# Optimization experiments

Measured on AMD Instinct MI355X. Metric: run time of the kernel, lower is better.

The kernel has to match this reference:

```python
import jax, jax.numpy as jnp
import numpy as np

D_K = 128

def setup_inputs() -> dict:
    key = jax.random.key(0)
    k1, k2, k3 = jax.random.split(key, 3)
    q = jax.random.normal(k1, (8192, D_K), dtype=jnp.float32)
    k = jax.random.normal(k2, (8192, D_K), dtype=jnp.float32)
    v = jax.random.normal(k3, (8192, D_K), dtype=jnp.float32)
    return {"q": q, "k": k, "v": v}

def reference(q, k, v):
    # scores: [S_q, S_k]
    scores = jnp.einsum('qd,kd->qk', q, k) / jnp.sqrt(jnp.float32(D_K))
    attn = jax.nn.softmax(scores, axis=-1)  # softmax over keys (torch default last dim)
    return jnp.einsum('qk,kd->qd', attn, v)
```

## Files before the change

### kernel.cpp

```cpp
#include <hip/hip_runtime.h>
#include <math.h>


typedef _Float16 f16x8 __attribute__((ext_vector_type(8)));
typedef float    f32x16 __attribute__((ext_vector_type(16)));

constexpr int S_LEN = 8192;
constexpr int D_K   = 128;
constexpr int NSLICE = 8;
constexpr int ITERS2 = (S_LEN / NSLICE) / 64;

constexpr size_t WS_L_OFF = 0;
constexpr size_t KV_OFF   = 262144;
constexpr size_t PART_OFF = KV_OFF + (size_t)256 * 16384;
constexpr size_t WS_NEED  = PART_OFF + (size_t)7 * S_LEN * D_K * 4;

#define CSCALE (0.08838834764831845f * 1.44269504088896340736f)

union UH8 { _Float16 h[8]; uint4 q; f16x8 v; };
union UF4 { unsigned u[4]; uint4 q; f16x8 v; };

__device__ inline void async16(const uint4* g, uint4* l) {
  __builtin_amdgcn_global_load_lds(
      (const __attribute__((address_space(1))) unsigned int*)g,
      (__attribute__((address_space(3))) unsigned int*)l, 16, 0, 0);
}

template <bool ZOUT>
__global__ __launch_bounds__(512) void attn_prep(const float* __restrict__ K,
                                                 const float* __restrict__ V,
                                                 float* __restrict__ out,
                                                 char* __restrict__ ws) {
  const int t = blockIdx.x * 512 + threadIdx.x;
  uint4* KVg = (uint4*)(ws + KV_OFF);
  if (t < 131072) {
    int kt = t >> 9, idx = t & 511;
    int lane = idx & 63, s = idx >> 6;
    int key = kt * 32 + (lane & 31);
    int d0  = s * 16 + (lane >> 5) * 8;
    const float4* src = (const float4*)(K + (size_t)key * D_K + d0);
    float4 a = src[0], b = src[1];
    float f[8] = {a.x, a.y, a.z, a.w, b.x, b.y, b.z, b.w};
    UH8 h;
    #pragma unroll
    for (int j = 0; j < 8; ++j) h.h[j] = (_Float16)f[j];
    KVg[(size_t)kt * 1024 + idx] = h.q;
  } else if (t < 262144) {
    int g = t - 131072;
    int kt = g >> 9, idx = g & 511;
    int lane = idx & 63, c = (idx >> 6) & 3, kstep = idx >> 8;
    int d  = c * 32 + (lane & 31);
    int kb = kt * 32 + kstep * 16 + (lane >> 5) * 8;
    UH8 h;
    #pragma unroll
    for (int j = 0; j < 8; ++j) h.h[j] = (_Float16)V[(size_t)(kb + j) * D_K + d];
    KVg[(size_t)kt * 1024 + 512 + idx] = h.q;
  } else if (ZOUT && t < 327680) {
    int i = t - 262144;
    float4 z = make_float4(0.f, 0.f, 0.f, 0.f);
    float4* o4 = (float4*)out;
    #pragma unroll
    for (int j = 0; j < 4; ++j) o4[(size_t)i * 4 + j] = z;
  } else if (ZOUT && t < 329728) {
    int i = t - 327680;
    ((float4*)(ws + WS_L_OFF))[i] = make_float4(0.f, 0.f, 0.f, 0.f);
  }
}

__device__ inline void softmax32(const f32x16& Sa, const f32x16& Sb,
                                 float& lsum, UF4& A0, UF4& A1) {
  unsigned pk[8];
  #pragma unroll
  for (int i = 0; i < 8; ++i) {
    float p0 = __builtin_amdgcn_exp2f(Sa[2 * i]     + Sb[2 * i]);
    float p1 = __builtin_amdgcn_exp2f(Sa[2 * i + 1] + Sb[2 * i + 1]);
    lsum += p0 + p1;
    pk[i] = __builtin_bit_cast(unsigned, __builtin_amdgcn_cvt_pkrtz(p0, p1));
  }
  auto r0 = __builtin_amdgcn_permlane32_swap((int)pk[0], (int)pk[2], false, false);
  auto r1 = __builtin_amdgcn_permlane32_swap((int)pk[1], (int)pk[3], false, false);
  auto r2 = __builtin_amdgcn_permlane32_swap((int)pk[4], (int)pk[6], false, false);
  auto r3 = __builtin_amdgcn_permlane32_swap((int)pk[5], (int)pk[7], false, false);
  A0.u[0] = (unsigned)r0[0]; A0.u[2] = (unsigned)r0[1];
  A0.u[1] = (unsigned)r1[0]; A0.u[3] = (unsigned)r1[1];
  A1.u[0] = (unsigned)r2[0]; A1.u[2] = (unsigned)r2[1];
  A1.u[1] = (unsigned)r3[0]; A1.u[3] = (unsigned)r3[1];
}

template <bool PARTIAL>
__global__ __launch_bounds__(256, 2)
void attn_main(const float* __restrict__ Qg, float* __restrict__ out,
               char* __restrict__ ws) {
  __shared__ uint4 KV[2][2048];

  const int tid   = threadIdx.x;
  const int wave  = tid >> 6;
  const int lane  = tid & 63;
  const int lrow  = lane & 31;
  const int lhalf = lane >> 5;

  const int blk = blockIdx.x;
  const int ks  = blk & 7;
  const int qb  = blk >> 3;
  const int qw  = qb * 128 + wave * 32;

  {
    const int delay = (int)(((unsigned)blk * 2654435761u) >> 28);
    for (int i = 0; i < delay; ++i) __builtin_amdgcn_s_sleep(2);
  }

  float* ws_l = (float*)(ws + WS_L_OFF);

  f16x8 qf[8];
  {
    const int q = qw + lrow;
    #pragma unroll
    for (int s = 0; s < 8; ++s) {
      const float4* src = (const float4*)(Qg + (size_t)q * D_K + s * 16 + lhalf * 8);
      float4 a = src[0], b = src[1];
      float f[8] = {a.x, a.y, a.z, a.w, b.x, b.y, b.z, b.w};
      UH8 h;
      #pragma unroll
      for (int j = 0; j < 8; ++j) h.h[j] = (_Float16)(f[j] * CSCALE);
      qf[s] = h.v;
    }
  }

  f32x16 O0{}, O1{}, O2{}, O3{};
  float lsum = 0.f;

  const uint4* KVg = (const uint4*)(ws + KV_OFF);

  {
    const size_t base = (size_t)ks * 32768;
    #pragma unroll
    for (int i = 0; i < 8; ++i)
      async16(KVg + base + i * 256 + tid, &KV[0][i * 256 + tid]);
  }

  for (int it = 0; it < ITERS2; ++it) {
    const int buf = it & 1;
    __syncthreads();

    if (it + 1 < ITERS2) {
      const size_t base = (size_t)ks * 32768 + (size_t)(it + 1) * 2048;
      #pragma unroll
      for (int i = 0; i < 8; ++i)
        async16(KVg + base + i * 256 + tid, &KV[buf ^ 1][i * 256 + tid]);
    }

    const uint4* sub0 = &KV[buf][0];
    const uint4* sub1 = &KV[buf][1024];

    f32x16 Sa0{}, Sb0{}, Sa1{}, Sb1{};
    __builtin_amdgcn_s_setprio(1);
    #pragma unroll
    for (int s = 0; s < 4; ++s) {
      f16x8 ka0 = __builtin_bit_cast(f16x8, sub0[(2 * s    ) * 64 + lane]);
      f16x8 kb0 = __builtin_bit_cast(f16x8, sub0[(2 * s + 1) * 64 + lane]);
      Sa0 = __builtin_amdgcn_mfma_f32_32x32x16_f16(ka0, qf[2 * s    ], Sa0, 0, 0, 0);
      Sb0 = __builtin_amdgcn_mfma_f32_32x32x16_f16(kb0, qf[2 * s + 1], Sb0, 0, 0, 0);
    }
    #pragma unroll
    for (int s = 0; s < 4; ++s) {
      f16x8 ka1 = __builtin_bit_cast(f16x8, sub1[(2 * s    ) * 64 + lane]);
      f16x8 kb1 = __builtin_bit_cast(f16x8, sub1[(2 * s + 1) * 64 + lane]);
      Sa1 = __builtin_amdgcn_mfma_f32_32x32x16_f16(ka1, qf[2 * s    ], Sa1, 0, 0, 0);
      Sb1 = __builtin_amdgcn_mfma_f32_32x32x16_f16(kb1, qf[2 * s + 1], Sb1, 0, 0, 0);
    }
    __builtin_amdgcn_s_setprio(0);

    UF4 A00, A01;
    softmax32(Sa0, Sb0, lsum, A00, A01);

    __builtin_amdgcn_s_setprio(1);
    #pragma unroll
    for (int kstep = 0; kstep < 2; ++kstep) {
      f16x8 pf = kstep ? A01.v : A00.v;
      f16x8 v0 = __builtin_bit_cast(f16x8, sub0[512 + kstep * 256 +   0 + lane]);
      f16x8 v1 = __builtin_bit_cast(f16x8, sub0[512 + kstep * 256 +  64 + lane]);
      f16x8 v2 = __builtin_bit_cast(f16x8, sub0[512 + kstep * 256 + 128 + lane]);
      f16x8 v3 = __builtin_bit_cast(f16x8, sub0[512 + kstep * 256 + 192 + lane]);
      O0 = __builtin_amdgcn_mfma_f32_32x32x16_f16(pf, v0, O0, 0, 0, 0);
      O1 = __builtin_amdgcn_mfma_f32_32x32x16_f16(pf, v1, O1, 0, 0, 0);
      O2 = __builtin_amdgcn_mfma_f32_32x32x16_f16(pf, v2, O2, 0, 0, 0);
      O3 = __builtin_amdgcn_mfma_f32_32x32x16_f16(pf, v3, O3, 0, 0, 0);
    }
    __builtin_amdgcn_s_setprio(0);

    UF4 A10, A11;
    softmax32(Sa1, Sb1, lsum, A10, A11);

    __builtin_amdgcn_s_setprio(1);
    #pragma unroll
    for (int kstep = 0; kstep < 2; ++kstep) {
      f16x8 pf = kstep ? A11.v : A10.v;
      f16x8 v0 = __builtin_bit_cast(f16x8, sub1[512 + kstep * 256 +   0 + lane]);
      f16x8 v1 = __builtin_bit_cast(f16x8, sub1[512 + kstep * 256 +  64 + lane]);
      f16x8 v2 = __builtin_bit_cast(f16x8, sub1[512 + kstep * 256 + 128 + lane]);
      f16x8 v3 = __builtin_bit_cast(f16x8, sub1[512 + kstep * 256 + 192 + lane]);
      O0 = __builtin_amdgcn_mfma_f32_32x32x16_f16(pf, v0, O0, 0, 0, 0);
      O1 = __builtin_amdgcn_mfma_f32_32x32x16_f16(pf, v1, O1, 0, 0, 0);
      O2 = __builtin_amdgcn_mfma_f32_32x32x16_f16(pf, v2, O2, 0, 0, 0);
      O3 = __builtin_amdgcn_mfma_f32_32x32x16_f16(pf, v3, O3, 0, 0, 0);
    }
    __builtin_amdgcn_s_setprio(0);
  }

  lsum += __shfl_xor(lsum, 32);

  if (PARTIAL) {
    if (lhalf == 0) ws_l[ks * S_LEN + qw + lrow] = lsum;
    float* obase = (ks == 0) ? out
                 : (float*)(ws + PART_OFF) + (size_t)(ks - 1) * S_LEN * D_K;
    #pragma unroll
    for (int r = 0; r < 16; ++r) {
      int row = (r & 3) + 8 * (r >> 2) + 4 * lhalf;
      float* dst = obase + (size_t)(qw + row) * D_K + lrow;
      dst[ 0] = O0[r];
      dst[32] = O1[r];
      dst[64] = O2[r];
      dst[96] = O3[r];
    }
  } else {
    if (lhalf == 0) atomicAdd(ws_l + qw + lrow, lsum);
    #pragma unroll
    for (int r = 0; r < 16; ++r) {
      int row = (r & 3) + 8 * (r >> 2) + 4 * lhalf;
      float* dst = out + (size_t)(qw + row) * D_K + lrow;
      atomicAdd(dst +  0, O0[r]);
      atomicAdd(dst + 32, O1[r]);
      atomicAdd(dst + 64, O2[r]);
      atomicAdd(dst + 96, O3[r]);
    }
  }
}

__global__ __launch_bounds__(256) void attn_norm(float* __restrict__ out,
                                                 const float* __restrict__ lpart,
                                                 const float* __restrict__ opart,
                                                 int nparts) {
  int i = blockIdx.x * 256 + threadIdx.x;
  int q = i >> 5;
  float4* o4 = (float4*)out;
  float4 acc = o4[i];
  float l = lpart[q];
  for (int s = 1; s <= nparts; ++s) {
    float4 p = ((const float4*)opart)[(size_t)(s - 1) * 262144 + i];
    acc.x += p.x; acc.y += p.y; acc.z += p.z; acc.w += p.w;
    l += lpart[s * S_LEN + q];
  }
  float inv = 1.0f / l;
  acc.x *= inv; acc.y *= inv; acc.z *= inv; acc.w *= inv;
  o4[i] = acc;
}

extern "C" void kernel_launch(void* const* d_in, const int* in_sizes, int n_in,
                              void* d_out, int out_size, void* d_ws, size_t ws_size,
                              hipStream_t stream) {
  const float* q = (const float*)d_in[0];
  const float* k = (const float*)d_in[1];
  const float* v = (const float*)d_in[2];
  float* out = (float*)d_out;
  char* ws = (char*)d_ws;

  if (ws_size >= WS_NEED) {
    attn_prep<false><<<dim3(512), dim3(512), 0, stream>>>(k, v, out, ws);
    attn_main<true><<<dim3(512), dim3(256), 0, stream>>>(q, out, ws);
    attn_norm<<<dim3(1024), dim3(256), 0, stream>>>(
        out, (const float*)(ws + WS_L_OFF), (const float*)(ws + PART_OFF), 7);
  } else {
    attn_prep<true><<<dim3(645), dim3(512), 0, stream>>>(k, v, out, ws);
    attn_main<false><<<dim3(512), dim3(256), 0, stream>>>(q, out, ws);
    attn_norm<<<dim3(1024), dim3(256), 0, stream>>>(
        out, (const float*)(ws + WS_L_OFF), (const float*)(ws + PART_OFF), 0);
  }
}
```

Measured before the change: 112.3 us.

## Use 8-wave blocks with triple-buffered LDS and staggered wave-group PV schedule

Doubles the block size to 512 threads covering 256 queries per block, halving the grid, and moves from double to triple buffering of the K/V tiles in LDS. The second group of four waves defers its second PV product to the next iteration, so its softmax and MFMA phases are offset from the first group and can interleave on the matrix units. The random sleep delay at kernel start is removed. This costs more LDS per block and more register pressure from the carried P fragments, and with only 256 blocks, occupancy and load balance may change.

```diff
diff --git a/kernel.cpp b/kernel.cpp
--- a/kernel.cpp
+++ b/kernel.cpp
@@ -67,6 +67,20 @@
   }
 }
 
+__device__ inline void qk32(const uint4* sub, const f16x8* qf, int lane,
+                            f32x16& Sa, f32x16& Sb) {
+  Sa = f32x16{}; Sb = f32x16{};
+  __builtin_amdgcn_s_setprio(1);
+  #pragma unroll
+  for (int s = 0; s < 4; ++s) {
+    f16x8 ka = __builtin_bit_cast(f16x8, sub[(2 * s    ) * 64 + lane]);
+    f16x8 kb = __builtin_bit_cast(f16x8, sub[(2 * s + 1) * 64 + lane]);
+    Sa = __builtin_amdgcn_mfma_f32_32x32x16_f16(ka, qf[2 * s    ], Sa, 0, 0, 0);
+    Sb = __builtin_amdgcn_mfma_f32_32x32x16_f16(kb, qf[2 * s + 1], Sb, 0, 0, 0);
+  }
+  __builtin_amdgcn_s_setprio(0);
+}
+
 __device__ inline void softmax32(const f32x16& Sa, const f32x16& Sb,
                                  float& lsum, UF4& A0, UF4& A1) {
   unsigned pk[8];
@@ -87,27 +101,41 @@
   A1.u[1] = (unsigned)r3[0]; A1.u[3] = (unsigned)r3[1];
 }
 
+__device__ inline void pv32(const uint4* sub, const UF4& A0, const UF4& A1,
+                            int lane, f32x16* O) {
+  __builtin_amdgcn_s_setprio(1);
+  #pragma unroll
+  for (int kstep = 0; kstep < 2; ++kstep) {
+    f16x8 pf = kstep ? A1.v : A0.v;
+    f16x8 v0 = __builtin_bit_cast(f16x8, sub[512 + kstep * 256 +   0 + lane]);
+    f16x8 v1 = __builtin_bit_cast(f16x8, sub[512 + kstep * 256 +  64 + lane]);
+    f16x8 v2 = __builtin_bit_cast(f16x8, sub[512 + kstep * 256 + 128 + lane]);
+    f16x8 v3 = __builtin_bit_cast(f16x8, sub[512 + kstep * 256 + 192 + lane]);
+    O[0] = __builtin_amdgcn_mfma_f32_32x32x16_f16(pf, v0, O[0], 0, 0, 0);
+    O[1] = __builtin_amdgcn_mfma_f32_32x32x16_f16(pf, v1, O[1], 0, 0, 0);
+    O[2] = __builtin_amdgcn_mfma_f32_32x32x16_f16(pf, v2, O[2], 0, 0, 0);
+    O[3] = __builtin_amdgcn_mfma_f32_32x32x16_f16(pf, v3, O[3], 0, 0, 0);
+  }
+  __builtin_amdgcn_s_setprio(0);
+}
+
 template <bool PARTIAL>
-__global__ __launch_bounds__(256, 2)
+__global__ __launch_bounds__(512, 2)
 void attn_main(const float* __restrict__ Qg, float* __restrict__ out,
                char* __restrict__ ws) {
-  __shared__ uint4 KV[2][2048];
+  __shared__ uint4 KV[3][2048];
 
   const int tid   = threadIdx.x;
   const int wave  = tid >> 6;
   const int lane  = tid & 63;
   const int lrow  = lane & 31;
   const int lhalf = lane >> 5;
+  const int g1    = wave >> 2;
 
   const int blk = blockIdx.x;
   const int ks  = blk & 7;
   const int qb  = blk >> 3;
-  const int qw  = qb * 128 + wave * 32;
-
-  {
-    const int delay = (int)(((unsigned)blk * 2654435761u) >> 28);
-    for (int i = 0; i < delay; ++i) __builtin_amdgcn_s_sleep(2);
-  }
+  const int qw  = qb * 256 + wave * 32;
 
   float* ws_l = (float*)(ws + WS_L_OFF);
 
@@ -126,7 +154,7 @@
     }
   }
 
-  f32x16 O0{}, O1{}, O2{}, O3{};
+  f32x16 O[4] = {f32x16{}, f32x16{}, f32x16{}, f32x16{}};
   float lsum = 0.f;
 
   const uint4* KVg = (const uint4*)(ws + KV_OFF);
@@ -134,78 +162,52 @@
   {
     const size_t base = (size_t)ks * 32768;
     #pragma unroll
-    for (int i = 0; i < 8; ++i)
-      async16(KVg + base + i * 256 + tid, &KV[0][i * 256 + tid]);
-  }
-
+    for (int i = 0; i < 4; ++i)
+      async16(KVg + base + i * 512 + tid, &KV[0][i * 512 + tid]);
+  }
+
+  UF4 A1c0, A1c1;
+  const uint4* sub1prev = &KV[0][1024];
+
+  int cur = 0, nxt = 1;
   for (int it = 0; it < ITERS2; ++it) {
-    const int buf = it & 1;
     __syncthreads();
 
     if (it + 1 < ITERS2) {
       const size_t base = (size_t)ks * 32768 + (size_t)(it + 1) * 2048;
       #pragma unroll
-      for (int i = 0; i < 8; ++i)
-        async16(KVg + base + i * 256 + tid, &KV[buf ^ 1][i * 256 + tid]);
-    }
-
-    const uint4* sub0 = &KV[buf][0];
-    const uint4* sub1 = &KV[buf][1024];
-
-    f32x16 Sa0{}, Sb0{}, Sa1{}, Sb1{};
-    __builtin_amdgcn_s_setprio(1);
-    #pragma unroll
-    for (int s = 0; s < 4; ++s) {
-      f16x8 ka0 = __builtin_bit_cast(f16x8, sub0[(2 * s    ) * 64 + lane]);
-      f16x8 kb0 = __builtin_bit_cast(f16x8, sub0[(2 * s + 1) * 64 + lane]);
-      Sa0 = __builtin_amdgcn_mfma_f32_32x32x16_f16(ka0, qf[2 * s    ], Sa0, 0, 0, 0);
-      Sb0 = __builtin_amdgcn_mfma_f32_32x32x16_f16(kb0, qf[2 * s + 1], Sb0, 0, 0, 0);
-    }
-    #pragma unroll
-    for (int s = 0; s < 4; ++s) {
-      f16x8 ka1 = __builtin_bit_cast(f16x8, sub1[(2 * s    ) * 64 + lane]);
-      f16x8 kb1 = __builtin_bit_cast(f16x8, sub1[(2 * s + 1) * 64 + lane]);
-      Sa1 = __builtin_amdgcn_mfma_f32_32x32x16_f16(ka1, qf[2 * s    ], Sa1, 0, 0, 0);
-      Sb1 = __builtin_amdgcn_mfma_f32_32x32x16_f16(kb1, qf[2 * s + 1], Sb1, 0, 0, 0);
-    }
-    __builtin_amdgcn_s_setprio(0);
-
-    UF4 A00, A01;
-    softmax32(Sa0, Sb0, lsum, A00, A01);
-
-    __builtin_amdgcn_s_setprio(1);
-    #pragma unroll
-    for (int kstep = 0; kstep < 2; ++kstep) {
-      f16x8 pf = kstep ? A01.v : A00.v;
-      f16x8 v0 = __builtin_bit_cast(f16x8, sub0[512 + kstep * 256 +   0 + lane]);
-      f16x8 v1 = __builtin_bit_cast(f16x8, sub0[512 + kstep * 256 +  64 + lane]);
-      f16x8 v2 = __builtin_bit_cast(f16x8, sub0[512 + kstep * 256 + 128 + lane]);
-      f16x8 v3 = __builtin_bit_cast(f16x8, sub0[512 + kstep * 256 + 192 + lane]);
-      O0 = __builtin_amdgcn_mfma_f32_32x32x16_f16(pf, v0, O0, 0, 0, 0);
-      O1 = __builtin_amdgcn_mfma_f32_32x32x16_f16(pf, v1, O1, 0, 0, 0);
-      O2 = __builtin_amdgcn_mfma_f32_32x32x16_f16(pf, v2, O2, 0, 0, 0);
-      O3 = __builtin_amdgcn_mfma_f32_32x32x16_f16(pf, v3, O3, 0, 0, 0);
-    }
-    __builtin_amdgcn_s_setprio(0);
-
-    UF4 A10, A11;
-    softmax32(Sa1, Sb1, lsum, A10, A11);
-
-    __builtin_amdgcn_s_setprio(1);
-    #pragma unroll
-    for (int kstep = 0; kstep < 2; ++kstep) {
-      f16x8 pf = kstep ? A11.v : A10.v;
-      f16x8 v0 = __builtin_bit_cast(f16x8, sub1[512 + kstep * 256 +   0 + lane]);
-      f16x8 v1 = __builtin_bit_cast(f16x8, sub1[512 + kstep * 256 +  64 + lane]);
-      f16x8 v2 = __builtin_bit_cast(f16x8, sub1[512 + kstep * 256 + 128 + lane]);
-      f16x8 v3 = __builtin_bit_cast(f16x8, sub1[512 + kstep * 256 + 192 + lane]);
-      O0 = __builtin_amdgcn_mfma_f32_32x32x16_f16(pf, v0, O0, 0, 0, 0);
-      O1 = __builtin_amdgcn_mfma_f32_32x32x16_f16(pf, v1, O1, 0, 0, 0);
-      O2 = __builtin_amdgcn_mfma_f32_32x32x16_f16(pf, v2, O2, 0, 0, 0);
-      O3 = __builtin_amdgcn_mfma_f32_32x32x16_f16(pf, v3, O3, 0, 0, 0);
-    }
-    __builtin_amdgcn_s_setprio(0);
-  }
+      for (int i = 0; i < 4; ++i)
+        async16(KVg + base + i * 512 + tid, &KV[nxt][i * 512 + tid]);
+    }
+
+    const uint4* sub0 = &KV[cur][0];
+    const uint4* sub1 = &KV[cur][1024];
+
+    if (!g1) {
+      f32x16 Sa, Sb;
+      UF4 A0, A1;
+      qk32(sub0, qf, lane, Sa, Sb);
+      softmax32(Sa, Sb, lsum, A0, A1);
+      pv32(sub0, A0, A1, lane, O);
+      qk32(sub1, qf, lane, Sa, Sb);
+      softmax32(Sa, Sb, lsum, A0, A1);
+      pv32(sub1, A0, A1, lane, O);
+    } else {
+      if (it) pv32(sub1prev, A1c0, A1c1, lane, O);
+      f32x16 Sa, Sb;
+      UF4 A0, A1;
+      qk32(sub0, qf, lane, Sa, Sb);
+      softmax32(Sa, Sb, lsum, A0, A1);
+      pv32(sub0, A0, A1, lane, O);
+      qk32(sub1, qf, lane, Sa, Sb);
+      softmax32(Sa, Sb, lsum, A1c0, A1c1);
+      sub1prev = sub1;
+    }
+
+    cur = nxt;
+    nxt = (nxt == 2) ? 0 : nxt + 1;
+  }
+  if (g1) pv32(sub1prev, A1c0, A1c1, lane, O);
 
   lsum += __shfl_xor(lsum, 32);
 
@@ -217,10 +219,10 @@
     for (int r = 0; r < 16; ++r) {
       int row = (r & 3) + 8 * (r >> 2) + 4 * lhalf;
       float* dst = obase + (size_t)(qw + row) * D_K + lrow;
-      dst[ 0] = O0[r];
-      dst[32] = O1[r];
-      dst[64] = O2[r];
-      dst[96] = O3[r];
+      dst[ 0] = O[0][r];
+      dst[32] = O[1][r];
+      dst[64] = O[2][r];
+      dst[96] = O[3][r];
     }
   } else {
     if (lhalf == 0) atomicAdd(ws_l + qw + lrow, lsum);
@@ -228,10 +230,10 @@
     for (int r = 0; r < 16; ++r) {
       int row = (r & 3) + 8 * (r >> 2) + 4 * lhalf;
       float* dst = out + (size_t)(qw + row) * D_K + lrow;
-      atomicAdd(dst +  0, O0[r]);
-      atomicAdd(dst + 32, O1[r]);
-      atomicAdd(dst + 64, O2[r]);
-      atomicAdd(dst + 96, O3[r]);
+      atomicAdd(dst +  0, O[0][r]);
+      atomicAdd(dst + 32, O[1][r]);
+      atomicAdd(dst + 64, O[2][r]);
+      atomicAdd(dst + 96, O[3][r]);
     }
   }
 }
@@ -266,12 +268,12 @@
 
   if (ws_size >= WS_NEED) {
     attn_prep<false><<<dim3(512), dim3(512), 0, stream>>>(k, v, out, ws);
-    attn_main<true><<<dim3(512), dim3(256), 0, stream>>>(q, out, ws);
+    attn_main<true><<<dim3(256), dim3(512), 0, stream>>>(q, out, ws);
     attn_norm<<<dim3(1024), dim3(256), 0, stream>>>(
         out, (const float*)(ws + WS_L_OFF), (const float*)(ws + PART_OFF), 7);
   } else {
     attn_prep<true><<<dim3(645), dim3(512), 0, stream>>>(k, v, out, ws);
-    attn_main<false><<<dim3(512), dim3(256), 0, stream>>>(q, out, ws);
+    attn_main<false><<<dim3(256), dim3(512), 0, stream>>>(q, out, ws);
     attn_norm<<<dim3(1024), dim3(256), 0, stream>>>(
         out, (const float*)(ws + WS_L_OFF), (const float*)(ws + PART_OFF), 0);
   }
```

After: 110.3 us. No clear change (-1.8%).

## Load first K subtile directly into registers and shrink LDS staging buffer

Applied to the files above, without the earlier changes.

The first K subtile of each iteration now goes straight from global memory into registers, prefetched one iteration ahead, so only the second K subtile and both V subtiles are staged through LDS. The LDS buffer shrinks from 2048 to 1536 uint4 per stage. The QK^T chains are also merged into a single accumulator per subtile instead of split Sa/Sb accumulators. This cuts LDS traffic and footprint but adds eight live f16x8 registers and longer serial MFMA dependency chains, which may add register pressure and latency.

```diff
diff --git a/kernel.cpp b/kernel.cpp
--- a/kernel.cpp
+++ b/kernel.cpp
@@ -67,13 +67,13 @@
   }
 }
 
-__device__ inline void softmax32(const f32x16& Sa, const f32x16& Sb,
+__device__ inline void softmax32(const f32x16& S,
                                  float& lsum, UF4& A0, UF4& A1) {
   unsigned pk[8];
   #pragma unroll
   for (int i = 0; i < 8; ++i) {
-    float p0 = __builtin_amdgcn_exp2f(Sa[2 * i]     + Sb[2 * i]);
-    float p1 = __builtin_amdgcn_exp2f(Sa[2 * i + 1] + Sb[2 * i + 1]);
+    float p0 = __builtin_amdgcn_exp2f(S[2 * i]);
+    float p1 = __builtin_amdgcn_exp2f(S[2 * i + 1]);
     lsum += p0 + p1;
     pk[i] = __builtin_bit_cast(unsigned, __builtin_amdgcn_cvt_pkrtz(p0, p1));
   }
@@ -91,7 +91,7 @@
 __global__ __launch_bounds__(256, 2)
 void attn_main(const float* __restrict__ Qg, float* __restrict__ out,
                char* __restrict__ ws) {
-  __shared__ uint4 KV[2][2048];
+  __shared__ uint4 KV[2][1536];
 
   const int tid   = threadIdx.x;
   const int wave  = tid >> 6;
@@ -130,57 +130,73 @@
   float lsum = 0.f;
 
   const uint4* KVg = (const uint4*)(ws + KV_OFF);
-
-  {
-    const size_t base = (size_t)ks * 32768;
-    #pragma unroll
-    for (int i = 0; i < 8; ++i)
-      async16(KVg + base + i * 256 + tid, &KV[0][i * 256 + tid]);
-  }
+  const size_t sbase = (size_t)ks * 32768;
+
+  #pragma unroll
+  for (int i = 0; i < 2; ++i)
+    async16(KVg + sbase + 1024 + i * 256 + tid, &KV[0][i * 256 + tid]);
+  #pragma unroll
+  for (int i = 0; i < 2; ++i)
+    async16(KVg + sbase + 512 + i * 256 + tid, &KV[0][512 + i * 256 + tid]);
+  #pragma unroll
+  for (int i = 0; i < 2; ++i)
+    async16(KVg + sbase + 1536 + i * 256 + tid, &KV[0][1024 + i * 256 + tid]);
+
+  f16x8 kA[8];
+  #pragma unroll
+  for (int s = 0; s < 8; ++s)
+    kA[s] = __builtin_bit_cast(f16x8, KVg[sbase + s * 64 + lane]);
 
   for (int it = 0; it < ITERS2; ++it) {
     const int buf = it & 1;
     __syncthreads();
 
+    const size_t nb = sbase + (size_t)(it + 1) * 2048;
     if (it + 1 < ITERS2) {
-      const size_t base = (size_t)ks * 32768 + (size_t)(it + 1) * 2048;
-      #pragma unroll
-      for (int i = 0; i < 8; ++i)
-        async16(KVg + base + i * 256 + tid, &KV[buf ^ 1][i * 256 + tid]);
-    }
-
-    const uint4* sub0 = &KV[buf][0];
-    const uint4* sub1 = &KV[buf][1024];
-
-    f32x16 Sa0{}, Sb0{}, Sa1{}, Sb1{};
-    __builtin_amdgcn_s_setprio(1);
-    #pragma unroll
-    for (int s = 0; s < 4; ++s) {
-      f16x8 ka0 = __builtin_bit_cast(f16x8, sub0[(2 * s    ) * 64 + lane]);
-      f16x8 kb0 = __builtin_bit_cast(f16x8, sub0[(2 * s + 1) * 64 + lane]);
-      Sa0 = __builtin_amdgcn_mfma_f32_32x32x16_f16(ka0, qf[2 * s    ], Sa0, 0, 0, 0);
-      Sb0 = __builtin_amdgcn_mfma_f32_32x32x16_f16(kb0, qf[2 * s + 1], Sb0, 0, 0, 0);
-    }
-    #pragma unroll
-    for (int s = 0; s < 4; ++s) {
-      f16x8 ka1 = __builtin_bit_cast(f16x8, sub1[(2 * s    ) * 64 + lane]);
-      f16x8 kb1 = __builtin_bit_cast(f16x8, sub1[(2 * s + 1) * 64 + lane]);
-      Sa1 = __builtin_amdgcn_mfma_f32_32x32x16_f16(ka1, qf[2 * s    ], Sa1, 0, 0, 0);
-      Sb1 = __builtin_amdgcn_mfma_f32_32x32x16_f16(kb1, qf[2 * s + 1], Sb1, 0, 0, 0);
+      #pragma unroll
+      for (int i = 0; i < 2; ++i)
+        async16(KVg + nb + 1024 + i * 256 + tid, &KV[buf ^ 1][i * 256 + tid]);
+      #pragma unroll
+      for (int i = 0; i < 2; ++i)
+        async16(KVg + nb + 512 + i * 256 + tid, &KV[buf ^ 1][512 + i * 256 + tid]);
+      #pragma unroll
+      for (int i = 0; i < 2; ++i)
+        async16(KVg + nb + 1536 + i * 256 + tid, &KV[buf ^ 1][1024 + i * 256 + tid]);
+    }
+
+    const uint4* sub = &KV[buf][0];
+
+    f32x16 S0{};
+    __builtin_amdgcn_s_setprio(1);
+    #pragma unroll
+    for (int s = 0; s < 8; ++s)
+      S0 = __builtin_amdgcn_mfma_f32_32x32x16_f16(kA[s], qf[s], S0, 0, 0, 0);
+    __builtin_amdgcn_s_setprio(0);
+
+    #pragma unroll
+    for (int s = 0; s < 8; ++s)
+      kA[s] = __builtin_bit_cast(f16x8, KVg[nb + s * 64 + lane]);
+
+    f32x16 S1{};
+    __builtin_amdgcn_s_setprio(1);
+    #pragma unroll
+    for (int s = 0; s < 8; ++s) {
+      f16x8 kb = __builtin_bit_cast(f16x8, sub[s * 64 + lane]);
+      S1 = __builtin_amdgcn_mfma_f32_32x32x16_f16(kb, qf[s], S1, 0, 0, 0);
     }
     __builtin_amdgcn_s_setprio(0);
 
     UF4 A00, A01;
-    softmax32(Sa0, Sb0, lsum, A00, A01);
+    softmax32(S0, lsum, A00, A01);
 
     __builtin_amdgcn_s_setprio(1);
     #pragma unroll
     for (int kstep = 0; kstep < 2; ++kstep) {
       f16x8 pf = kstep ? A01.v : A00.v;
-      f16x8 v0 = __builtin_bit_cast(f16x8, sub0[512 + kstep * 256 +   0 + lane]);
-      f16x8 v1 = __builtin_bit_cast(f16x8, sub0[512 + kstep * 256 +  64 + lane]);
-      f16x8 v2 = __builtin_bit_cast(f16x8, sub0[512 + kstep * 256 + 128 + lane]);
-      f16x8 v3 = __builtin_bit_cast(f16x8, sub0[512 + kstep * 256 + 192 + lane]);
+      f16x8 v0 = __builtin_bit_cast(f16x8, sub[512 + kstep * 256 +   0 + lane]);
+      f16x8 v1 = __builtin_bit_cast(f16x8, sub[512 + kstep * 256 +  64 + lane]);
+      f16x8 v2 = __builtin_bit_cast(f16x8, sub[512 + kstep * 256 + 128 + lane]);
+      f16x8 v3 = __builtin_bit_cast(f16x8, sub[512 + kstep * 256 + 192 + lane]);
       O0 = __builtin_amdgcn_mfma_f32_32x32x16_f16(pf, v0, O0, 0, 0, 0);
       O1 = __builtin_amdgcn_mfma_f32_32x32x16_f16(pf, v1, O1, 0, 0, 0);
       O2 = __builtin_amdgcn_mfma_f32_32x32x16_f16(pf, v2, O2, 0, 0, 0);
@@ -189,16 +205,16 @@
     __builtin_amdgcn_s_setprio(0);
 
     UF4 A10, A11;
-    softmax32(Sa1, Sb1, lsum, A10, A11);
+    softmax32(S1, lsum, A10, A11);
 
     __builtin_amdgcn_s_setprio(1);
     #pragma unroll
     for (int kstep = 0; kstep < 2; ++kstep) {
       f16x8 pf = kstep ? A11.v : A10.v;
-      f16x8 v0 = __builtin_bit_cast(f16x8, sub1[512 + kstep * 256 +   0 + lane]);
-      f16x8 v1 = __builtin_bit_cast(f16x8, sub1[512 + kstep * 256 +  64 + lane]);
-      f16x8 v2 = __builtin_bit_cast(f16x8, sub1[512 + kstep * 256 + 128 + lane]);
-      f16x8 v3 = __builtin_bit_cast(f16x8, sub1[512 + kstep * 256 + 192 + lane]);
+      f16x8 v0 = __builtin_bit_cast(f16x8, sub[1024 + kstep * 256 +   0 + lane]);
+      f16x8 v1 = __builtin_bit_cast(f16x8, sub[1024 + kstep * 256 +  64 + lane]);
+      f16x8 v2 = __builtin_bit_cast(f16x8, sub[1024 + kstep * 256 + 128 + lane]);
+      f16x8 v3 = __builtin_bit_cast(f16x8, sub[1024 + kstep * 256 + 192 + lane]);
       O0 = __builtin_amdgcn_mfma_f32_32x32x16_f16(pf, v0, O0, 0, 0, 0);
       O1 = __builtin_amdgcn_mfma_f32_32x32x16_f16(pf, v1, O1, 0, 0, 0);
       O2 = __builtin_amdgcn_mfma_f32_32x32x16_f16(pf, v2, O2, 0, 0, 0);
```

Measured after the change: 114.2 us. Within noise of the previous version (+1.7%).
